# Kernel tuning notes

Measured on AMD Instinct MI355X. Metric: run time of the kernel, lower is better.

The kernel has to match this reference:

```python
import jax, jax.numpy as jnp
import numpy as np

N = 50000
E = 1600000
IN_CH = 34
HID = 64
OUT = 64
NEG_SLOPE = 0.2


def _gat_layer(x, src, dst, W, a_src, a_dst, bias, heads, out_ch, concat):
    n = x.shape[0]
    xw = (x @ W).reshape(n, heads, out_ch)                      # [N,H,C]
    al_src = jnp.sum(xw * a_src[None], axis=-1)                  # [N,H]
    al_dst = jnp.sum(xw * a_dst[None], axis=-1)                  # [N,H]
    e = jax.nn.leaky_relu(al_src[src] + al_dst[dst], NEG_SLOPE)  # [E,H]
    # segment softmax over incoming edges of each dst node (self-loops ensure non-empty)
    m = jax.ops.segment_max(e, dst, num_segments=n)              # [N,H]
    ex = jnp.exp(e - m[dst])
    denom = jax.ops.segment_sum(ex, dst, num_segments=n)         # [N,H]
    alpha = ex / denom[dst]                                      # [E,H]
    msg = xw[src] * alpha[:, :, None]                            # [E,H,C]
    out = jax.ops.segment_sum(msg, dst, num_segments=n)          # [N,H,C]
    if concat:
        out = out.reshape(n, heads * out_ch)
    else:
        out = out.mean(axis=1)
    return out + bias


def setup_inputs() -> dict:
    key = jax.random.key(0)
    ks = jax.random.split(key, 12)
    x = jax.random.normal(ks[0], (N, IN_CH), dtype=jnp.float32)
    edge_index = jax.random.randint(ks[1], (2, E), 0, N, dtype=jnp.int64)
    # layer 1: heads=2, concat -> 128
    W1 = jax.random.normal(ks[2], (IN_CH, 2 * HID), dtype=jnp.float32) * 0.1
    a_src1 = jax.random.normal(ks[3], (2, HID), dtype=jnp.float32) * 0.1
    a_dst1 = jax.random.normal(ks[4], (2, HID), dtype=jnp.float32) * 0.1
    b1 = jnp.zeros((2 * HID,), dtype=jnp.float32)
    # layer 2: heads=1, mean
    W2 = jax.random.normal(ks[5], (2 * HID, OUT), dtype=jnp.float32) * 0.1
    a_src2 = jax.random.normal(ks[6], (1, OUT), dtype=jnp.float32) * 0.1
    a_dst2 = jax.random.normal(ks[7], (1, OUT), dtype=jnp.float32) * 0.1
    b2 = jnp.zeros((OUT,), dtype=jnp.float32)
    return {"x": x, "edge_index": edge_index, "W1": W1, "a_src1": a_src1,
            "a_dst1": a_dst1, "b1": b1, "W2": W2, "a_src2": a_src2,
            "a_dst2": a_dst2, "b2": b2}


def reference(x, edge_index, W1, a_src1, a_dst1, b1, W2, a_src2, a_dst2, b2):
    n = x.shape[0]
    loops = jnp.arange(n, dtype=edge_index.dtype)
    src = jnp.concatenate([edge_index[0], loops])  # PyG GATConv add_self_loops=True
    dst = jnp.concatenate([edge_index[1], loops])
    h = _gat_layer(x, src, dst, W1, a_src1, a_dst1, b1, heads=2, out_ch=HID, concat=True)
    h = jax.nn.relu(h)
    out = _gat_layer(h, src, dst, W2, a_src2, a_dst2, b2, heads=1, out_ch=OUT, concat=False)
    return out
```

## Files before the change

### kernel.cpp

```cpp
#include <hip/hip_runtime.h>
#include <math.h>

#define N_NODES 50000
#define E_EDGES 1600000
#define IN_CH   34
#define NEG     0.2f
#define NB      196
#define CAP     10000

typedef __attribute__((ext_vector_type(2))) float fv2;

static __device__ __forceinline__ unsigned short f2bf(float f) {
    unsigned int u = __float_as_uint(f);
    u += 0x7fffu + ((u >> 16) & 1u);
    return (unsigned short)(u >> 16);
}
static __device__ __forceinline__ float bflo(unsigned int u) {
    return __uint_as_float(u << 16);
}
static __device__ __forceinline__ float bfhi(unsigned int u) {
    return __uint_as_float(u & 0xffff0000u);
}
static __device__ __forceinline__ float lrelu_exp(float e) {
    return expf(e > 0.f ? e : NEG * e);
}

static __device__ __forceinline__ int scan256_1024(int v, int* wsum) {
    const int lane = threadIdx.x & 63, wv = threadIdx.x >> 6;
    int x = v;
    #pragma unroll
    for (int off = 1; off < 64; off <<= 1) {
        int y = __shfl_up(x, off);
        if (lane >= off) x += y;
    }
    if (wv < 4 && lane == 63) wsum[wv] = x;
    __syncthreads();
    if (threadIdx.x < 4) {
        int s = wsum[threadIdx.x];
        #pragma unroll
        for (int off = 1; off < 4; off <<= 1) {
            int y = __shfl_up(s, off);
            if ((int)threadIdx.x >= off) s += y;
        }
        wsum[threadIdx.x] = s;
    }
    __syncthreads();
    const int woff = (wv >= 1 && wv < 4) ? wsum[wv - 1] : 0;
    return woff + x - v;
}

__global__ __launch_bounds__(1024) void k_bin(
    const int* __restrict__ srcA, const int* __restrict__ dstA,
    int* __restrict__ gcur, unsigned int* __restrict__ binned)
{
    __shared__ unsigned int raw[8192];
    __shared__ unsigned int ebuf[8192];
    __shared__ int cnt[256], loff[256], lcur[256], cur[256];
    __shared__ int wsum[4];
    const int tid = threadIdx.x;
    const int base = blockIdx.x * 8192;
    const int mE = min(8192, E_EDGES - base);
    const int nq = mE >> 2;
    if (tid < 256) cnt[tid] = 0;
    __syncthreads();
    for (int q = tid; q < nq; q += 1024) {
        const int4 d4 = ((const int4*)(dstA + base))[q];
        const int4 s4 = ((const int4*)(srcA + base))[q];
        raw[4 * q + 0] = ((unsigned)d4.x << 16) | (unsigned)s4.x;
        raw[4 * q + 1] = ((unsigned)d4.y << 16) | (unsigned)s4.y;
        raw[4 * q + 2] = ((unsigned)d4.z << 16) | (unsigned)s4.z;
        raw[4 * q + 3] = ((unsigned)d4.w << 16) | (unsigned)s4.w;
        atomicAdd(&cnt[d4.x >> 8], 1);
        atomicAdd(&cnt[d4.y >> 8], 1);
        atomicAdd(&cnt[d4.z >> 8], 1);
        atomicAdd(&cnt[d4.w >> 8], 1);
    }
    __syncthreads();
    const int v = (tid < 256) ? cnt[tid] : 0;
    const int excl = scan256_1024(v, wsum);
    if (tid < 256) { loff[tid] = excl; lcur[tid] = excl; }
    if (tid < NB) cur[tid] = (v > 0) ? (tid * CAP + atomicAdd(&gcur[tid], v)) : 0;
    __syncthreads();
    for (int p = tid; p < mE; p += 1024) {
        const unsigned int u = raw[p];
        const int q = atomicAdd(&lcur[u >> 24], 1);
        ebuf[q] = u;
    }
    __syncthreads();
    for (int p = tid; p < mE; p += 1024) {
        const unsigned int u = ebuf[p];
        const int b = (int)(u >> 24);
        binned[cur[b] + (p - loff[b])] = u;
    }
}

__global__ __launch_bounds__(256) void k_node1(
    const float* __restrict__ x, const float* __restrict__ W1,
    const float* __restrict__ a_src, const float* __restrict__ a_dst,
    unsigned short* __restrict__ xw1b,
    float* __restrict__ al_s, float* __restrict__ al_d)
{
    __shared__ float sW[IN_CH * 132];
    __shared__ float sx[32 * 35];
    __shared__ float sas[128], sad[128];
    const int tid = threadIdx.x;
    for (int i = tid; i < IN_CH * 128; i += 256) {
        int k = i >> 7, c = i & 127;
        sW[k * 132 + c] = W1[i];
    }
    if (tid < 128) { sas[tid] = a_src[tid]; sad[tid] = a_dst[tid]; }
    const int n0 = blockIdx.x * 32;
    for (int i = tid; i < 32 * IN_CH; i += 256) {
        int n = i / IN_CH;
        sx[n * 35 + (i - n * IN_CH)] = (n0 + n < N_NODES) ? x[n0 * IN_CH + i] : 0.f;
    }
    __syncthreads();

    const int tc = tid & 31, tn = tid >> 5;
    float acc[4][4] = {{0.f}};
    for (int k = 0; k < IN_CH; ++k) {
        const float4 wv = *reinterpret_cast<const float4*>(&sW[k * 132 + 4 * tc]);
        #pragma unroll
        for (int j = 0; j < 4; ++j) {
            const float hj = sx[(4 * tn + j) * 35 + k];
            acc[j][0] += hj * wv.x; acc[j][1] += hj * wv.y;
            acc[j][2] += hj * wv.z; acc[j][3] += hj * wv.w;
        }
    }
    #pragma unroll
    for (int j = 0; j < 4; ++j) {
        const int node = n0 + 4 * tn + j;
        float ps = 0.f, pd = 0.f;
        #pragma unroll
        for (int c = 0; c < 4; ++c) {
            ps += acc[j][c] * sas[4 * tc + c];
            pd += acc[j][c] * sad[4 * tc + c];
        }
        #pragma unroll
        for (int off = 1; off < 16; off <<= 1) {
            ps += __shfl_xor(ps, off);
            pd += __shfl_xor(pd, off);
        }
        if (node < N_NODES) {
            if ((tc & 15) == 0) {
                int h = tc >> 4;
                al_s[node * 2 + h] = ps;
                al_d[node * 2 + h] = pd;
            }
            ushort4 u;
            u.x = f2bf(acc[j][0]); u.y = f2bf(acc[j][1]);
            u.z = f2bf(acc[j][2]); u.w = f2bf(acc[j][3]);
            *reinterpret_cast<ushort4*>(&xw1b[node * 128 + 4 * tc]) = u;
        }
    }
}

__global__ __launch_bounds__(1024) void k_fine(
    const int* __restrict__ gcur, const unsigned int* __restrict__ binned,
    int2* __restrict__ rowspan, int* __restrict__ sorted_src)
{
    __shared__ unsigned int sbin[CAP];
    __shared__ int cnt[256], lcur[256];
    __shared__ int wsum[4];
    const int tid = threadIdx.x;
    const int b = blockIdx.x;
    const int bbase = b * CAP;
    const int cntb = gcur[b];
    if (tid < 256) cnt[tid] = 0;
    __syncthreads();
    for (int p = tid; p < cntb; p += 1024) {
        const unsigned int u = binned[bbase + p];
        sbin[p] = u;
        atomicAdd(&cnt[(u >> 16) & 255], 1);
    }
    __syncthreads();
    const int v = (tid < 256) ? cnt[tid] : 0;
    const int excl = scan256_1024(v, wsum);
    if (tid < 256) {
        lcur[tid] = excl;
        const int node = b * 256 + tid;
        if (node < N_NODES) rowspan[node] = make_int2(bbase + excl, bbase + excl + v);
    }
    __syncthreads();
    for (int p = tid; p < cntb; p += 1024) {
        const unsigned int u = sbin[p];
        const int q = atomicAdd(&lcur[(u >> 16) & 255], 1);
        sorted_src[bbase + q] = (int)(u & 0xffffu);
    }
}

__global__ __launch_bounds__(256) void k_gather1(
    const int2* __restrict__ rowspan, const int* __restrict__ sorted_src,
    const unsigned int* __restrict__ xw1u,
    const float* __restrict__ al_s, const float* __restrict__ al_d,
    const float* __restrict__ b1, float* __restrict__ hbuf)
{
    __shared__ float4 AB[2][4][32];
    const int wave = threadIdx.x >> 6;
    const int lane = threadIdx.x & 63;
    const int node = (blockIdx.x * 256 + threadIdx.x) >> 6;
    if (node >= N_NODES) return;
    const int2 span = rowspan[node];
    const int head = lane >> 5;

    const float2 ald  = *reinterpret_cast<const float2*>(&al_d[node * 2]);
    const float2 als0 = *reinterpret_cast<const float2*>(&al_s[node * 2]);
    const float w0h0 = lrelu_exp(als0.x + ald.x);
    const float w0h1 = lrelu_exp(als0.y + ald.y);
    const float wself = head ? w0h1 : w0h0;

    const unsigned int su = xw1u[node * 64 + lane];
    fv2 accX = { wself * bflo(su), wself * bfhi(su) };
    fv2 accY = { 0.f, 0.f };
    float dv0 = 0.f, dv1 = 0.f;
    const float4* ABh = AB[head][wave];

    for (int base = span.x; base < span.y; base += 64) {
        const int rem = span.y - base;
        const int m = rem < 64 ? rem : 64;
        const int mp = (m + 1) & ~1;
        if (lane < m) {
            const int s = sorted_src[base + lane];
            const float2 als = *reinterpret_cast<const float2*>(&al_s[s * 2]);
            const float w0 = lrelu_exp(als.x + ald.x);
            const float w1 = lrelu_exp(als.y + ald.y);
            dv0 += w0; dv1 += w1;
            const float offf = __int_as_float(s << 6);
            ((float2*)&AB[0][wave][lane >> 1])[lane & 1] = make_float2(offf, w0);
            ((float2*)&AB[1][wave][lane >> 1])[lane & 1] = make_float2(offf, w1);
        } else if (lane < mp) {
            const float offf = __int_as_float(node << 6);
            ((float2*)&AB[0][wave][lane >> 1])[lane & 1] = make_float2(offf, 0.f);
            ((float2*)&AB[1][wave][lane >> 1])[lane & 1] = make_float2(offf, 0.f);
        }
        const int P = mp >> 1;
        int p = 0;
        for (; p + 4 <= P; p += 4) {
            const float4 q0 = ABh[p + 0];
            const float4 q1 = ABh[p + 1];
            const float4 q2 = ABh[p + 2];
            const float4 q3 = ABh[p + 3];
            const unsigned int a0 = xw1u[__float_as_int(q0.x) + lane];
            const unsigned int b0 = xw1u[__float_as_int(q0.z) + lane];
            const unsigned int a1 = xw1u[__float_as_int(q1.x) + lane];
            const unsigned int b1v = xw1u[__float_as_int(q1.z) + lane];
            const unsigned int a2 = xw1u[__float_as_int(q2.x) + lane];
            const unsigned int b2 = xw1u[__float_as_int(q2.z) + lane];
            const unsigned int a3 = xw1u[__float_as_int(q3.x) + lane];
            const unsigned int b3 = xw1u[__float_as_int(q3.z) + lane];
            fv2 f;
            f.x = bflo(a0); f.y = bfhi(a0); accX += f * q0.y;
            f.x = bflo(b0); f.y = bfhi(b0); accY += f * q0.w;
            f.x = bflo(a1); f.y = bfhi(a1); accX += f * q1.y;
            f.x = bflo(b1v); f.y = bfhi(b1v); accY += f * q1.w;
            f.x = bflo(a2); f.y = bfhi(a2); accX += f * q2.y;
            f.x = bflo(b2); f.y = bfhi(b2); accY += f * q2.w;
            f.x = bflo(a3); f.y = bfhi(a3); accX += f * q3.y;
            f.x = bflo(b3); f.y = bfhi(b3); accY += f * q3.w;
        }
        for (; p < P; ++p) {
            const float4 q = ABh[p];
            const unsigned int a = xw1u[__float_as_int(q.x) + lane];
            const unsigned int b = xw1u[__float_as_int(q.z) + lane];
            fv2 f;
            f.x = bflo(a); f.y = bfhi(a); accX += f * q.y;
            f.x = bflo(b); f.y = bfhi(b); accY += f * q.w;
        }
    }
    accX += accY;
    #pragma unroll
    for (int off = 32; off; off >>= 1) {
        dv0 += __shfl_xor(dv0, off);
        dv1 += __shfl_xor(dv1, off);
    }
    const float den = head ? (dv1 + w0h1) : (dv0 + w0h0);
    const float2 bv = *reinterpret_cast<const float2*>(&b1[2 * lane]);
    float o0 = accX.x / den + bv.x;
    float o1 = accX.y / den + bv.y;
    o0 = o0 > 0.f ? o0 : 0.f;
    o1 = o1 > 0.f ? o1 : 0.f;
    *reinterpret_cast<float2*>(&hbuf[node * 128 + 2 * lane]) = make_float2(o0, o1);
}

__global__ __launch_bounds__(256) void k_node2(
    const float* __restrict__ hbuf, const float* __restrict__ W2,
    const float* __restrict__ a_src, const float* __restrict__ a_dst,
    unsigned short* __restrict__ xw2b, float* __restrict__ al_s, float* __restrict__ al_d)
{
    __shared__ float sW[128 * 64];
    __shared__ float sh[64 * 129];
    __shared__ float sas[64], sad[64];
    const int tid = threadIdx.x;
    for (int i = tid; i < 128 * 64; i += 256) sW[i] = W2[i];
    if (tid < 64) { sas[tid] = a_src[tid]; sad[tid] = a_dst[tid]; }
    const int n0 = blockIdx.x * 64;
    for (int i = tid; i < 64 * 128; i += 256) {
        int n = i >> 7, c = i & 127;
        sh[n * 129 + c] = (n0 + n < N_NODES) ? hbuf[(long)(n0 + n) * 128 + c] : 0.f;
    }
    __syncthreads();

    const int tc = tid & 15, tn = tid >> 4;
    float acc[4][4] = {{0.f}};
    for (int k = 0; k < 128; ++k) {
        const float4 wv = *reinterpret_cast<const float4*>(&sW[k * 64 + 4 * tc]);
        #pragma unroll
        for (int j = 0; j < 4; ++j) {
            const float hj = sh[(4 * tn + j) * 129 + k];
            acc[j][0] += hj * wv.x; acc[j][1] += hj * wv.y;
            acc[j][2] += hj * wv.z; acc[j][3] += hj * wv.w;
        }
    }
    #pragma unroll
    for (int j = 0; j < 4; ++j) {
        const int node = n0 + 4 * tn + j;
        float ps = 0.f, pd = 0.f;
        #pragma unroll
        for (int c = 0; c < 4; ++c) {
            ps += acc[j][c] * sas[4 * tc + c];
            pd += acc[j][c] * sad[4 * tc + c];
        }
        #pragma unroll
        for (int off = 1; off < 16; off <<= 1) {
            ps += __shfl_xor(ps, off);
            pd += __shfl_xor(pd, off);
        }
        if (node < N_NODES) {
            if (tc == 0) { al_s[node] = ps; al_d[node] = pd; }
            ushort4 u;
            u.x = f2bf(acc[j][0]); u.y = f2bf(acc[j][1]);
            u.z = f2bf(acc[j][2]); u.w = f2bf(acc[j][3]);
            *reinterpret_cast<ushort4*>(&xw2b[node * 64 + 4 * tc]) = u;
        }
    }
}

__global__ __launch_bounds__(256) void k_gather2(
    const int2* __restrict__ rowspan, const int* __restrict__ sorted_src,
    const unsigned int* __restrict__ xw2u,
    const float* __restrict__ al_s, const float* __restrict__ al_d,
    const float* __restrict__ b2, float* __restrict__ out)
{
    __shared__ float4 AB[4][32];
    const int wave = threadIdx.x >> 6;
    const int lane = threadIdx.x & 63;
    const int node = (blockIdx.x * 256 + threadIdx.x) >> 6;
    if (node >= N_NODES) return;
    const int2 span = rowspan[node];
    const int li = lane & 31, hsel = lane >> 5;

    const float ald = al_d[node];
    const float w0s = lrelu_exp(al_s[node] + ald);
    const unsigned int su = xw2u[node * 32 + li];
    const float wself = hsel ? 0.f : w0s;
    fv2 acc = { wself * bflo(su), wself * bfhi(su) };
    float dv = 0.f;
    const float4* ABw = AB[wave];

    for (int base = span.x; base < span.y; base += 64) {
        const int rem = span.y - base;
        const int m = rem < 64 ? rem : 64;
        const int mp = (m + 3) & ~3;
        if (lane < m) {
            const int s = sorted_src[base + lane];
            const float w = lrelu_exp(al_s[s] + ald);
            dv += w;
            ((float2*)&AB[wave][lane >> 1])[lane & 1] =
                make_float2(__int_as_float(s << 5), w);
        } else if (lane < mp) {
            ((float2*)&AB[wave][lane >> 1])[lane & 1] =
                make_float2(__int_as_float(node << 5), 0.f);
        }
        const int P = mp >> 1;
        int p = hsel;
        for (; p + 2 < P; p += 4) {
            const float4 qA = ABw[p];
            const float4 qB = ABw[p + 2];
            const unsigned int aA = xw2u[__float_as_int(qA.x) + li];
            const unsigned int bA = xw2u[__float_as_int(qA.z) + li];
            const unsigned int aB = xw2u[__float_as_int(qB.x) + li];
            const unsigned int bB = xw2u[__float_as_int(qB.z) + li];
            fv2 f;
            f.x = bflo(aA); f.y = bfhi(aA); acc += f * qA.y;
            f.x = bflo(bA); f.y = bfhi(bA); acc += f * qA.w;
            f.x = bflo(aB); f.y = bfhi(aB); acc += f * qB.y;
            f.x = bflo(bB); f.y = bfhi(bB); acc += f * qB.w;
        }
        for (; p < P; p += 2) {
            const float4 q = ABw[p];
            const unsigned int a = xw2u[__float_as_int(q.x) + li];
            const unsigned int b = xw2u[__float_as_int(q.z) + li];
            fv2 f;
            f.x = bflo(a); f.y = bfhi(a); acc += f * q.y;
            f.x = bflo(b); f.y = bfhi(b); acc += f * q.w;
        }
    }
    acc.x += __shfl_xor(acc.x, 32);
    acc.y += __shfl_xor(acc.y, 32);
    #pragma unroll
    for (int off = 32; off; off >>= 1) dv += __shfl_xor(dv, off);
    if (lane < 32) {
        const float den = dv + w0s;
        const float2 bv = *reinterpret_cast<const float2*>(&b2[2 * li]);
        *reinterpret_cast<float2*>(&out[node * 64 + 2 * li]) =
            make_float2(acc.x / den + bv.x, acc.y / den + bv.y);
    }
}

extern "C" void kernel_launch(void* const* d_in, const int* in_sizes, int n_in,
                              void* d_out, int out_size, void* d_ws, size_t ws_size,
                              hipStream_t stream)
{
    const float* x   = (const float*)d_in[0];
    const int*   ei  = (const int*)d_in[1];
    const float* W1  = (const float*)d_in[2];
    const float* as1 = (const float*)d_in[3];
    const float* ad1 = (const float*)d_in[4];
    const float* b1  = (const float*)d_in[5];
    const float* W2  = (const float*)d_in[6];
    const float* as2 = (const float*)d_in[7];
    const float* ad2 = (const float*)d_in[8];
    const float* b2  = (const float*)d_in[9];
    float* out = (float*)d_out;

    const int* srcA = ei;
    const int* dstA = ei + E_EDGES;

    char* ws = (char*)d_ws;
    int2*  rowspan    = (int2*)(ws);
    int*   sorted_src = (int*)(ws + 409600);
    int*   gcur       = (int*)(ws + 8249600);
    float* al_s1      = (float*)(ws + 8251648);
    float* al_d1      = (float*)(ws + 8651648);
    float* al_s2      = (float*)(ws + 9051648);
    float* al_d2      = (float*)(ws + 9251648);
    unsigned short* xw1b = (unsigned short*)(ws + 9451648);
    float* hbuf       = (float*)(ws + 22251648);
    unsigned int* binned = (unsigned int*)hbuf;
    unsigned short* xw2b = (unsigned short*)(ws + 47851648);

    hipMemsetAsync(gcur, 0, NB * sizeof(int), stream);
    hipLaunchKernelGGL(k_bin, dim3(NB), dim3(1024), 0, stream,
                       srcA, dstA, gcur, binned);
    hipLaunchKernelGGL(k_node1, dim3((N_NODES + 31) / 32), dim3(256), 0, stream,
                       x, W1, as1, ad1, xw1b, al_s1, al_d1);
    hipLaunchKernelGGL(k_fine, dim3(NB), dim3(1024), 0, stream,
                       gcur, binned, rowspan, sorted_src);
    hipLaunchKernelGGL(k_gather1, dim3((N_NODES + 3) / 4), dim3(256), 0, stream,
                       rowspan, sorted_src, (const unsigned int*)xw1b,
                       al_s1, al_d1, b1, hbuf);
    hipLaunchKernelGGL(k_node2, dim3((N_NODES + 63) / 64), dim3(256), 0, stream,
                       hbuf, W2, as2, ad2, xw2b, al_s2, al_d2);
    hipLaunchKernelGGL(k_gather2, dim3((N_NODES + 3) / 4), dim3(256), 0, stream,
                       rowspan, sorted_src, (const unsigned int*)xw2b,
                       al_s2, al_d2, b2, out);
}
```

Before: 262.9 us.

## Replace shared-memory atomic histograms with wave-ballot match grouping in binning sorts

Both counting-sort kernels (coarse binning and fine per-node sort) now group lanes with equal keys using 8 ballots per wave and keep per-wave histograms. Only one leader lane per group updates the counter, which removes shared-memory atomics and their contention. The fine sort also stages sorted entries in shared memory so the global write of sorted_src becomes coalesced and ordering is deterministic. The cost is extra ballot work per element, 16x larger histogram storage, and per-wave prefix loops.

```diff
diff --git a/kernel.cpp b/kernel.cpp
--- a/kernel.cpp
+++ b/kernel.cpp
@@ -23,6 +23,16 @@
 }
 static __device__ __forceinline__ float lrelu_exp(float e) {
     return expf(e > 0.f ? e : NEG * e);
+}
+
+static __device__ __forceinline__ unsigned long long grp8(int key, bool valid) {
+    unsigned long long m = __ballot(valid);
+    #pragma unroll
+    for (int b = 0; b < 8; ++b) {
+        const unsigned long long bal = __ballot(key & (1 << b));
+        m &= (key & (1 << b)) ? bal : ~bal;
+    }
+    return m;
 }
 
 static __device__ __forceinline__ int scan256_1024(int v, int* wsum) {
@@ -55,38 +65,71 @@
 {
     __shared__ unsigned int raw[8192];
     __shared__ unsigned int ebuf[8192];
-    __shared__ int cnt[256], loff[256], lcur[256], cur[256];
+    __shared__ int pcnt[16][256];
+    __shared__ int loff[256], cur[256];
     __shared__ int wsum[4];
     const int tid = threadIdx.x;
+    const int wave = tid >> 6, lane = tid & 63;
+    const unsigned long long below = (1ull << lane) - 1ull;
     const int base = blockIdx.x * 8192;
     const int mE = min(8192, E_EDGES - base);
-    const int nq = mE >> 2;
-    if (tid < 256) cnt[tid] = 0;
-    __syncthreads();
-    for (int q = tid; q < nq; q += 1024) {
-        const int4 d4 = ((const int4*)(dstA + base))[q];
-        const int4 s4 = ((const int4*)(srcA + base))[q];
-        raw[4 * q + 0] = ((unsigned)d4.x << 16) | (unsigned)s4.x;
-        raw[4 * q + 1] = ((unsigned)d4.y << 16) | (unsigned)s4.y;
-        raw[4 * q + 2] = ((unsigned)d4.z << 16) | (unsigned)s4.z;
-        raw[4 * q + 3] = ((unsigned)d4.w << 16) | (unsigned)s4.w;
-        atomicAdd(&cnt[d4.x >> 8], 1);
-        atomicAdd(&cnt[d4.y >> 8], 1);
-        atomicAdd(&cnt[d4.z >> 8], 1);
-        atomicAdd(&cnt[d4.w >> 8], 1);
-    }
-    __syncthreads();
-    const int v = (tid < 256) ? cnt[tid] : 0;
-    const int excl = scan256_1024(v, wsum);
-    if (tid < 256) { loff[tid] = excl; lcur[tid] = excl; }
-    if (tid < NB) cur[tid] = (v > 0) ? (tid * CAP + atomicAdd(&gcur[tid], v)) : 0;
-    __syncthreads();
-    for (int p = tid; p < mE; p += 1024) {
-        const unsigned int u = raw[p];
-        const int q = atomicAdd(&lcur[u >> 24], 1);
-        ebuf[q] = u;
-    }
-    __syncthreads();
+
+    for (int i = tid; i < 16 * 256; i += 1024) ((int*)pcnt)[i] = 0;
+    __syncthreads();
+
+    for (int c = wave; c < 128; c += 16) {
+        const int idx = c * 64 + lane;
+        const bool valid = idx < mE;
+        unsigned int u = 0;
+        if (valid) {
+            const int d = dstA[base + idx], s = srcA[base + idx];
+            u = ((unsigned)d << 16) | (unsigned)s;
+            raw[idx] = u;
+        }
+        const int key = (int)(u >> 24);
+        const unsigned long long m = grp8(key, valid);
+        if (valid && (m & below) == 0ull)
+            pcnt[wave][key] += (int)__popcll(m);
+    }
+    __syncthreads();
+
+    int run = 0;
+    if (tid < 256) {
+        #pragma unroll 1
+        for (int w = 0; w < 16; ++w) {
+            const int t = pcnt[w][tid];
+            pcnt[w][tid] = run;
+            run += t;
+        }
+    }
+    const int excl = scan256_1024(run, wsum);
+    if (tid < 256) loff[tid] = excl;
+    if (tid < NB) cur[tid] = (run > 0) ? (tid * CAP + atomicAdd(&gcur[tid], run)) : 0;
+    __syncthreads();
+    if (tid < 256) {
+        #pragma unroll 1
+        for (int w = 0; w < 16; ++w) pcnt[w][tid] += excl;
+    }
+    __syncthreads();
+
+    for (int c = wave; c < 128; c += 16) {
+        const int idx = c * 64 + lane;
+        const bool valid = idx < mE;
+        const unsigned int u = valid ? raw[idx] : 0u;
+        const int key = (int)(u >> 24);
+        const unsigned long long m = grp8(key, valid);
+        const int rank = (int)__popcll(m & below);
+        const int leader = valid ? (__ffsll((long long)m) - 1) : 0;
+        int basep = 0;
+        if (valid && rank == 0) basep = pcnt[wave][key];
+        basep = __shfl(basep, leader);
+        if (valid) {
+            ebuf[basep + rank] = u;
+            if (rank == 0) pcnt[wave][key] = basep + (int)__popcll(m);
+        }
+    }
+    __syncthreads();
+
     for (int p = tid; p < mE; p += 1024) {
         const unsigned int u = ebuf[p];
         const int b = (int)(u >> 24);
@@ -160,32 +203,71 @@
     int2* __restrict__ rowspan, int* __restrict__ sorted_src)
 {
     __shared__ unsigned int sbin[CAP];
-    __shared__ int cnt[256], lcur[256];
+    __shared__ unsigned int ssrt[CAP];
+    __shared__ int pcnt[16][256];
     __shared__ int wsum[4];
     const int tid = threadIdx.x;
+    const int wave = tid >> 6, lane = tid & 63;
+    const unsigned long long below = (1ull << lane) - 1ull;
     const int b = blockIdx.x;
     const int bbase = b * CAP;
     const int cntb = gcur[b];
-    if (tid < 256) cnt[tid] = 0;
-    __syncthreads();
+    const int nch = (cntb + 63) >> 6;
+
+    for (int i = tid; i < 16 * 256; i += 1024) ((int*)pcnt)[i] = 0;
+    __syncthreads();
+
+    for (int c = wave; c < nch; c += 16) {
+        const int idx = c * 64 + lane;
+        const bool valid = idx < cntb;
+        unsigned int u = 0;
+        if (valid) { u = binned[bbase + idx]; sbin[idx] = u; }
+        const int key = (int)((u >> 16) & 255u);
+        const unsigned long long m = grp8(key, valid);
+        if (valid && (m & below) == 0ull)
+            pcnt[wave][key] += (int)__popcll(m);
+    }
+    __syncthreads();
+
+    int run = 0;
+    if (tid < 256) {
+        #pragma unroll 1
+        for (int w = 0; w < 16; ++w) {
+            const int t = pcnt[w][tid];
+            pcnt[w][tid] = run;
+            run += t;
+        }
+    }
+    const int excl = scan256_1024(run, wsum);
+    if (tid < 256) {
+        const int node = b * 256 + tid;
+        if (node < N_NODES)
+            rowspan[node] = make_int2(bbase + excl, bbase + excl + run);
+        #pragma unroll 1
+        for (int w = 0; w < 16; ++w) pcnt[w][tid] += excl;
+    }
+    __syncthreads();
+
+    for (int c = wave; c < nch; c += 16) {
+        const int idx = c * 64 + lane;
+        const bool valid = idx < cntb;
+        const unsigned int u = valid ? sbin[idx] : 0u;
+        const int key = (int)((u >> 16) & 255u);
+        const unsigned long long m = grp8(key, valid);
+        const int rank = (int)__popcll(m & below);
+        const int leader = valid ? (__ffsll((long long)m) - 1) : 0;
+        int basep = 0;
+        if (valid && rank == 0) basep = pcnt[wave][key];
+        basep = __shfl(basep, leader);
+        if (valid) {
+            ssrt[basep + rank] = u;
+            if (rank == 0) pcnt[wave][key] = basep + (int)__popcll(m);
+        }
+    }
+    __syncthreads();
+
     for (int p = tid; p < cntb; p += 1024) {
-        const unsigned int u = binned[bbase + p];
-        sbin[p] = u;
-        atomicAdd(&cnt[(u >> 16) & 255], 1);
-    }
-    __syncthreads();
-    const int v = (tid < 256) ? cnt[tid] : 0;
-    const int excl = scan256_1024(v, wsum);
-    if (tid < 256) {
-        lcur[tid] = excl;
-        const int node = b * 256 + tid;
-        if (node < N_NODES) rowspan[node] = make_int2(bbase + excl, bbase + excl + v);
-    }
-    __syncthreads();
-    for (int p = tid; p < cntb; p += 1024) {
-        const unsigned int u = sbin[p];
-        const int q = atomicAdd(&lcur[(u >> 16) & 255], 1);
-        sorted_src[bbase + q] = (int)(u & 0xffffu);
+        sorted_src[bbase + p] = (int)(ssrt[p] & 0xffffu);
     }
 }
 
```

Result: slower. 276.4 us (+5.1%).
